# Optimization experiments

Hardware: AMD Instinct MI355X
Metric: run time of the kernel (lower is better)

## Reference

```python
import jax, jax.numpy as jnp
import numpy as np

EPS = 1e-5
NUM_HEADS = 8


def _conv_transpose_3x3_s2(x, w):
    # x: [B,Cin,H,W], w: [Cin,Cout,3,3] (torch ConvTranspose2d layout), stride 2, no padding
    # output spatial = (H-1)*2 + 3 = 2H+1
    return jax.lax.conv_transpose(
        x, w, strides=(2, 2), padding='VALID',
        dimension_numbers=('NCHW', 'IOHW', 'NCHW'))


def setup_inputs() -> dict:
    key = jax.random.key(0)
    ks = jax.random.split(key, 8)
    B, C, H, W = 4, 256, 32, 32
    Co, Dk, Dv = 128, 64, 64
    s = 0.05
    return {
        'x': jax.random.normal(ks[0], (B, C, H, W), jnp.float32),
        'gamma': jnp.ones((C,), jnp.float32),
        'beta': jnp.zeros((C,), jnp.float32),
        'running_mean': jax.random.normal(ks[1], (C,), jnp.float32) * 0.1,
        'running_var': jax.random.uniform(ks[2], (C,), jnp.float32, 0.5, 1.5),
        'w_sc': jax.random.normal(ks[3], (C, Co, 3, 3), jnp.float32) * s,
        'w_q': jax.random.normal(ks[4], (C, Dk, 3, 3), jnp.float32) * s,
        'w_k': jax.random.normal(ks[5], (Dk, C), jnp.float32) * s,
        'w_v': jax.random.normal(ks[6], (Dv, C), jnp.float32) * s,
        'w_o': jax.random.normal(ks[7], (Co, Dv), jnp.float32) * s,
    }


def reference(x, gamma, beta, running_mean, running_var, w_sc, w_q, w_k, w_v, w_o):
    B, C, H, W = x.shape
    h = NUM_HEADS
    # BatchNorm (inference, running stats) + ReLU, shared by both branches
    inv = jax.lax.rsqrt(running_var + EPS)
    xn = (x - running_mean[None, :, None, None]) * (gamma * inv)[None, :, None, None] \
         + beta[None, :, None, None]
    xr = jax.nn.relu(xn)

    # Shortcut: ConvTranspose2d(C->Co, 3, stride 2) -> [B,Co,2H+1,2W+1]
    shortcut = _conv_transpose_3x3_s2(xr, w_sc)

    # Attention branch ('UP'): query upsampled via ConvTranspose, k/v 1x1 at low res
    q = _conv_transpose_3x3_s2(xr, w_q)              # [B,Dk,Hu,Wu]
    k = jnp.einsum('dc,bchw->bdhw', w_k, xr)         # [B,Dk,H,W]
    v = jnp.einsum('dc,bchw->bdhw', w_v, xr)         # [B,Dv,H,W]
    Hu, Wu = q.shape[2], q.shape[3]
    Nq, Nk = Hu * Wu, H * W
    Dk, Dv = q.shape[1], v.shape[1]
    dk = Dk // h
    qh = q.reshape(B, h, dk, Nq)
    kh = k.reshape(B, h, dk, Nk)
    vh = v.reshape(B, h, Dv // h, Nk)
    scores = jnp.einsum('bhdq,bhdk->bhqk', qh, kh) / jnp.sqrt(jnp.float32(dk))
    attn = jax.nn.softmax(scores, axis=-1)           # use_softmax=True
    out = jnp.einsum('bhqk,bhdk->bhdq', attn, vh)    # [B,h,dv,Nq]
    out = out.reshape(B, Dv, Hu, Wu)
    out = jnp.einsum('od,bdhw->bohw', w_o, out)      # 1x1 output projection -> Co

    return shortcut + out
```

## Files before the change

kernel.cpp:

```cpp
#include <hip/hip_runtime.h>

typedef unsigned short u16;
typedef unsigned int u32;

typedef float f4 __attribute__((ext_vector_type(4)));
typedef short s8v __attribute__((ext_vector_type(8)));
typedef u16 us8 __attribute__((ext_vector_type(8)));
typedef _Float16 h4 __attribute__((ext_vector_type(4)));
typedef __fp16 g2 __attribute__((ext_vector_type(2)));

__device__ __forceinline__ u16 f2bf(float x){ u32 b=__float_as_uint(x); b += 0x7FFFu + ((b>>16)&1u); return (u16)(b>>16); }
__device__ __forceinline__ u16 f2h(float x){ union{_Float16 h; u16 u;} c; c.h=(_Float16)x; return c.u; }

#define O_XRT  4096u
#define O_WPT  (O_XRT + 2367488u)
#define O_QH   (O_WPT + 884736u)
#define O_KT   (O_QH  + 2163200u)
#define O_V    (O_KT  + 524288u)
#define O_ATT  (O_V   + 524288u)
#define O_WKV  (O_ATT + 2163200u)
#define O_WO2  (O_WKV + 65536u)

__global__ __launch_bounds__(256) void k_prep(
    const float* __restrict__ x, const float* __restrict__ gamma, const float* __restrict__ beta,
    const float* __restrict__ mean, const float* __restrict__ var,
    const float* __restrict__ w_sc, const float* __restrict__ w_q,
    const float* __restrict__ w_k, const float* __restrict__ w_v, const float* __restrict__ w_o,
    u16* __restrict__ xrTp, u16* __restrict__ wpt,
    u16* __restrict__ wkv, u16* __restrict__ wo2)
{
  __shared__ float SS[128], SH[128];
  __shared__ __align__(16) u16 T[32*136];
  int bi = blockIdx.x, tid = threadIdx.x;
  if (bi < 256) {
    int b = bi >> 6, pt = (bi >> 1) & 31, ch = bi & 1;
    int pix0 = pt*32, c0 = ch*128;
    if (tid < 128) {
      int c = c0 + tid;
      float s = gamma[c]*rsqrtf(var[c] + 1e-5f);
      SS[tid] = s; SH[tid] = beta[c] - mean[c]*s;
    }
    __syncthreads();
    int pix_l = tid & 31, c_l = tid >> 5;
    #pragma unroll 4
    for (int it = 0; it < 16; ++it) {
      int cl = it*8 + c_l;
      float v = x[(((size_t)(b*256 + c0 + cl))<<10) + pix0 + pix_l];
      T[pix_l*136 + cl] = f2bf(fmaxf(v*SS[cl] + SH[cl], 0.f));
    }
    __syncthreads();
    int pix_r = tid >> 3, j = tid & 7;
    us8 v0 = *(const us8*)(T + pix_r*136 + j*8);
    us8 v1 = *(const us8*)(T + pix_r*136 + 64 + j*8);
    u16* dst = xrTp + (((size_t)(b*1156 + (pt+1)*34 + 1 + pix_r))<<8) + c0;
    *(us8*)(dst + j*8) = v0;
    *(us8*)(dst + 64 + j*8) = v1;
    return;
  }
  int wid = (bi - 256)*256 + tid;
  if (wid < 442368) {
    int c, m, ky, kx; float val;
    if (wid < 294912) {
      c = wid / 1152; int r = wid - c*1152; m = r / 9; int t9 = r - m*9; ky = t9/3; kx = t9 - ky*3;
      val = w_sc[wid];
    } else {
      int i2 = wid - 294912;
      c = i2 / 576; int r = i2 - c*576; m = r / 9; int t9 = r - m*9; ky = t9/3; kx = t9 - ky*3;
      val = w_q[i2] * 0.51007023f;
      m += 128;
    }
    int py = (ky==1) ? 1 : 0; int dy = (ky==0) ? 1 : 0;
    int px = (kx==1) ? 1 : 0; int dx = (kx==0) ? 1 : 0;
    int cls = py*2 + px;
    int tt, KP, base;
    if (cls==0){ tt = dy*2+dx; KP=1024; base=0; }
    else if (cls==1){ tt = dy; KP=512; base=196608; }
    else if (cls==2){ tt = dx; KP=512; base=294912; }
    else { tt = 0; KP=256; base=393216; }
    wpt[base + m*KP + tt*256 + c] = f2bf(val);
  } else if (wid < 475136) {
    int i = wid - 442368; int m = i >> 8, c = i & 255;
    float vv = (m < 64) ? w_k[m*256 + c] : w_v[(m-64)*256 + c];
    wkv[m*256 + c] = f2bf(vv);
  } else if (wid < 483328) {
    int i = wid - 475136;
    wo2[i] = f2bf(w_o[i]);
  } else if (wid < 500224) {
    int i = wid - 483328;
    int b = i / 4224; int r = i - b*4224;
    int hp = r >> 5, j = r & 31;
    int p;
    if (hp < 34) p = hp;
    else if (hp < 68) p = 33*34 + (hp - 34);
    else if (hp < 100) p = (hp - 68 + 1)*34;
    else p = (hp - 100 + 1)*34 + 33;
    *(us8*)(xrTp + (((size_t)(b*1156 + p))<<8) + j*8) = (us8)0;
  }
}

template<int PY,int PX,int TT>
__device__ __forceinline__ void conv_cls(
    const u16* __restrict__ xrTp, const u16* __restrict__ wcls,
    float* __restrict__ outF, u16* __restrict__ qh,
    int mb, int nb, u16* Blds)
{
  constexpr int Hy = 33 - PY, Wx = 33 - PX;
  constexpr int NC = 4*Hy*Wx;
  constexpr int KP = TT*256;
  constexpr int NKT = KP/64;
  int tid = threadIdx.x;
  int lane = tid & 63, wv = tid >> 6, quad = lane >> 4, c15 = lane & 15;
  int sn = tid >> 2, sg = tid & 3;
  int n_g = nb*64 + sn;
  int ncl = n_g < NC ? n_g : NC-1;
  int bb = ncl/(Hy*Wx); int rem = ncl - bb*(Hy*Wx); int yq = rem/Wx; int xq = rem - yq*Wx;
  const u16* bsrc = xrTp + (((size_t)(bb*1156 + (yq+1)*34 + xq+1))<<8) + sg*16;
  f4 acc[4];
  #pragma unroll
  for (int i=0;i<4;i++) acc[i] = (f4){0.f,0.f,0.f,0.f};
  const u16* arow = wcls + (size_t)(mb*64 + wv*16 + c15)*KP + quad*8;
  auto loadB = [&](int kt, us8& v0, us8& v1) {
    int tt = kt >> 2, c0 = (kt & 3)*64;
    int dy, dx;
    if (TT==4){ dy = tt>>1; dx = tt&1; }
    else if (TT==2){ if (PX==1){ dy=tt; dx=0; } else { dy=0; dx=tt; } }
    else { dy=0; dx=0; }
    const u16* p = bsrc - (((dy*34+dx))<<8) + c0;
    v0 = *(const us8*)p;
    v1 = *(const us8*)(p+8);
  };
  us8 cv0, cv1; loadB(0, cv0, cv1);
  int pb = 0;
  for (int kt = 0; kt < NKT; ++kt) {
    u16* Bw = Blds + pb*4608;
    *(us8*)(Bw + sn*72 + sg*16) = cv0;
    *(us8*)(Bw + sn*72 + sg*16 + 8) = cv1;
    __syncthreads();
    if (kt + 1 < NKT) loadB(kt+1, cv0, cv1);
    s8v a0 = *(const s8v*)(arow + kt*64);
    s8v a1 = *(const s8v*)(arow + kt*64 + 32);
    #pragma unroll
    for (int t4=0;t4<4;t4++) {
      const u16* br = Blds + pb*4608 + (t4*16 + c15)*72 + quad*8;
      s8v bf0 = *(const s8v*)br;
      s8v bf1 = *(const s8v*)(br + 32);
      acc[t4] = __builtin_amdgcn_mfma_f32_16x16x32_bf16(a0, bf0, acc[t4], 0, 0, 0);
      acc[t4] = __builtin_amdgcn_mfma_f32_16x16x32_bf16(a1, bf1, acc[t4], 0, 0, 0);
    }
    pb ^= 1;
  }
  #pragma unroll
  for (int t4=0;t4<4;t4++) {
    int n2 = nb*64 + t4*16 + c15;
    if (n2 < NC) {
      int bb2 = n2/(Hy*Wx); int rem2 = n2 - bb2*(Hy*Wx); int yq2 = rem2/Wx; int xq2 = rem2 - yq2*Wx;
      int pix = (2*yq2 + PY)*65 + (2*xq2 + PX);
      if (mb < 2) {
        int mrow = mb*64 + wv*16 + quad*4;
        #pragma unroll
        for (int rg=0; rg<4; rg++)
          outF[(size_t)(bb2*128 + mrow + rg)*4225 + pix] = acc[t4][rg];
      } else {
        int dv = wv*16 + quad*4;
        u16 pk[4];
        #pragma unroll
        for (int rg=0; rg<4; rg++) pk[rg] = f2h(acc[t4][rg]);
        *(uint2*)(qh + (((size_t)(bb2*4225 + pix))<<6) + dv) = *(uint2*)pk;
      }
    }
  }
}

__global__ __launch_bounds__(256) void k_conv(
    const u16* __restrict__ xrTp, const u16* __restrict__ wpt, const u16* __restrict__ wkv,
    float* __restrict__ outF, u16* __restrict__ qh,
    u16* __restrict__ kT, u16* __restrict__ vbuf)
{
  __shared__ __align__(16) u16 Blds[2*4608];
  int bi = blockIdx.x;
  if (bi < 795) {
    int mb = bi % 3, cy = bi / 3;
    if (cy < 69)       conv_cls<0,0,4>(xrTp, wpt,          outF, qh, mb, cy,     Blds);
    else if (cy < 135) conv_cls<0,1,2>(xrTp, wpt + 196608, outF, qh, mb, cy-69,  Blds);
    else if (cy < 201) conv_cls<1,0,2>(xrTp, wpt + 294912, outF, qh, mb, cy-135, Blds);
    else               conv_cls<1,1,1>(xrTp, wpt + 393216, outF, qh, mb, cy-201, Blds);
    return;
  }
  int t = bi - 795;
  int mb = t & 1, nb = t >> 1;
  int tid = threadIdx.x;
  int lane = tid & 63, wv = tid >> 6, quad = lane >> 4, c15 = lane & 15;
  int sn = tid >> 2, sg = tid & 3;
  int n_g = nb*64 + sn;
  int b0 = n_g >> 10, pix0 = n_g & 1023, y0 = pix0 >> 5, x0 = pix0 & 31;
  const u16* bsrc = xrTp + (((size_t)(b0*1156 + (y0+1)*34 + x0+1))<<8) + sg*16;
  f4 acc[4];
  #pragma unroll
  for (int i=0;i<4;i++) acc[i] = (f4){0.f,0.f,0.f,0.f};
  const u16* arow = wkv + (size_t)(mb*64 + wv*16 + c15)*256 + quad*8;
  us8 cv0 = *(const us8*)bsrc, cv1 = *(const us8*)(bsrc + 8);
  int pb = 0;
  for (int kt = 0; kt < 4; ++kt) {
    u16* Bw = Blds + pb*4608;
    *(us8*)(Bw + sn*72 + sg*16) = cv0;
    *(us8*)(Bw + sn*72 + sg*16 + 8) = cv1;
    __syncthreads();
    if (kt < 3) { cv0 = *(const us8*)(bsrc + (kt+1)*64); cv1 = *(const us8*)(bsrc + (kt+1)*64 + 8); }
    s8v a0 = *(const s8v*)(arow + kt*64);
    s8v a1 = *(const s8v*)(arow + kt*64 + 32);
    #pragma unroll
    for (int t4=0;t4<4;t4++) {
      const u16* br = Blds + pb*4608 + (t4*16 + c15)*72 + quad*8;
      s8v bf0 = *(const s8v*)br;
      s8v bf1 = *(const s8v*)(br + 32);
      acc[t4] = __builtin_amdgcn_mfma_f32_16x16x32_bf16(a0, bf0, acc[t4], 0, 0, 0);
      acc[t4] = __builtin_amdgcn_mfma_f32_16x16x32_bf16(a1, bf1, acc[t4], 0, 0, 0);
    }
    pb ^= 1;
  }
  int ml = wv*16 + quad*4;
  #pragma unroll
  for (int t4=0;t4<4;t4++) {
    int n2 = nb*64 + t4*16 + c15;
    int b = n2 >> 10, pix = n2 & 1023;
    if (mb == 0) {
      int h = ml >> 3, d0 = ml & 7;
      u16 pk[4];
      #pragma unroll
      for (int rg=0; rg<4; rg++) pk[rg] = f2h(acc[t4][rg]);
      *(uint2*)(kT + ((size_t)(b*8+h)<<13) + pix*8 + d0) = *(uint2*)pk;
    } else {
      #pragma unroll
      for (int rg=0; rg<4; rg++)
        vbuf[(((size_t)(b*64 + ml + rg))<<10) + pix] = f2h(acc[t4][rg]);
    }
  }
}

__global__ __launch_bounds__(256) void k_attn(
    const u16* __restrict__ qh, const u16* __restrict__ kT, const u16* __restrict__ vbuf,
    u16* __restrict__ attT)
{
  __shared__ __align__(16) u16 KL[8192];
  __shared__ __align__(16) u16 VL[9*1032];
  int qt = blockIdx.x, bh = blockIdx.y;
  int b = bh >> 3, h = bh & 7;
  int tid = threadIdx.x, lane = tid & 63, wv = tid >> 6, quad = lane >> 4, c15 = lane & 15;
  {
    const uint4* kg = (const uint4*)(kT + ((size_t)bh << 13));
    for (int i = tid; i < 1024; i += 256) ((uint4*)KL)[i] = kg[i];
    const u16* vg = vbuf + ((size_t)(b*64 + h*8) << 10);
    for (int i = tid; i < 1024; i += 256) {
      int dv = i >> 7, k8 = (i & 127) << 3;
      *(uint4*)(VL + dv*1032 + k8) = *(const uint4*)(vg + (dv<<10) + k8);
    }
    if (tid < 129) {
      us8 ones;
      #pragma unroll
      for (int i=0;i<8;i++) ones[i] = 0x3C00;
      *(us8*)(VL + 8*1032 + tid*8) = ones;
    }
  }
  __syncthreads();
  int q0 = qt*128 + wv*32 + c15;
  int q1 = q0 + 16;
  int qa = q0 < 4224 ? q0 : 4224;
  int qb = q1 < 4224 ? q1 : 4224;
  uint2 t0 = *(const uint2*)(qh + (((size_t)(b*4225 + qa))<<6) + h*8 + (quad&1)*4);
  uint2 t1 = *(const uint2*)(qh + (((size_t)(b*4225 + qb))<<6) + h*8 + (quad&1)*4);
  h4 bq0 = quad < 2 ? *(h4*)&t0 : (h4)(_Float16)0.f;
  h4 bq1 = quad < 2 ? *(h4*)&t1 : (h4)(_Float16)0.f;
  const u16* klb = KL + c15*8 + (quad&1)*4;
  int vr = c15 > 8 ? 8 : c15;
  const u16* vlb = VL + vr*1032 + quad*4;
  const f4 zf = {0.f,0.f,0.f,0.f};
  f4 O0 = {0.f,0.f,0.f,0.f}, O1 = {0.f,0.f,0.f,0.f};
  union HU { uint2 u; h4 h; };
  #pragma unroll 8
  for (int kt=0; kt<64; ++kt) {
    h4 ak = *(const h4*)(klb + kt*128);
    h4 av = *(const h4*)(vlb + kt*16);
    f4 s0 = __builtin_amdgcn_mfma_f32_16x16x16f16(ak, bq0, zf, 0, 0, 0);
    f4 s1 = __builtin_amdgcn_mfma_f32_16x16x16f16(ak, bq1, zf, 0, 0, 0);
    g2 p0l = __builtin_amdgcn_cvt_pkrtz(__builtin_amdgcn_exp2f(s0[0]), __builtin_amdgcn_exp2f(s0[1]));
    g2 p0h = __builtin_amdgcn_cvt_pkrtz(__builtin_amdgcn_exp2f(s0[2]), __builtin_amdgcn_exp2f(s0[3]));
    g2 p1l = __builtin_amdgcn_cvt_pkrtz(__builtin_amdgcn_exp2f(s1[0]), __builtin_amdgcn_exp2f(s1[1]));
    g2 p1h = __builtin_amdgcn_cvt_pkrtz(__builtin_amdgcn_exp2f(s1[2]), __builtin_amdgcn_exp2f(s1[3]));
    HU u0; u0.u.x = __builtin_bit_cast(u32, p0l); u0.u.y = __builtin_bit_cast(u32, p0h);
    HU u1; u1.u.x = __builtin_bit_cast(u32, p1l); u1.u.y = __builtin_bit_cast(u32, p1h);
    O0 = __builtin_amdgcn_mfma_f32_16x16x16f16(av, u0.h, O0, 0, 0, 0);
    O1 = __builtin_amdgcn_mfma_f32_16x16x16f16(av, u1.h, O1, 0, 0, 0);
  }
  float l0 = __shfl(O0[0], 32 + c15, 64);
  float l1 = __shfl(O1[0], 32 + c15, 64);
  float r0 = __builtin_amdgcn_rcpf(l0);
  float r1 = __builtin_amdgcn_rcpf(l1);
  if (quad < 2) {
    if (q0 < 4225) {
      u16 pk[4];
      #pragma unroll
      for (int rg=0;rg<4;rg++) pk[rg] = f2bf(O0[rg]*r0);
      *(uint2*)(attT + (((size_t)(b*4225 + q0))<<6) + h*8 + quad*4) = *(uint2*)pk;
    }
    if (q1 < 4225) {
      u16 pk[4];
      #pragma unroll
      for (int rg=0;rg<4;rg++) pk[rg] = f2bf(O1[rg]*r1);
      *(uint2*)(attT + (((size_t)(b*4225 + q1))<<6) + h*8 + quad*4) = *(uint2*)pk;
    }
  }
}

__global__ __launch_bounds__(256) void k_proj(
    const u16* __restrict__ attT, const u16* __restrict__ wo2, float* __restrict__ outF)
{
  int nbi = blockIdx.x, b = blockIdx.y;
  int tid = threadIdx.x;
  int lane = tid & 63, wv = tid >> 6, quad = lane >> 4, c15 = lane & 15;
  f4 acc[2][4];
  #pragma unroll
  for (int am=0;am<2;am++)
    #pragma unroll
    for (int i=0;i<4;i++) acc[am][i] = (f4){0.f,0.f,0.f,0.f};
  #pragma unroll
  for (int kt = 0; kt < 2; ++kt) {
    s8v a0 = *(const s8v*)(wo2 + (size_t)(wv*32 + c15)*64 + kt*32 + quad*8);
    s8v a1 = *(const s8v*)(wo2 + (size_t)(wv*32 + 16 + c15)*64 + kt*32 + quad*8);
    #pragma unroll
    for (int t4=0;t4<4;t4++) {
      int n = nbi*64 + t4*16 + c15;
      int nc = n < 4224 ? n : 4224;
      s8v bf = *(const s8v*)(attT + (((size_t)(b*4225 + nc))<<6) + kt*32 + quad*8);
      acc[0][t4] = __builtin_amdgcn_mfma_f32_16x16x32_bf16(a0, bf, acc[0][t4], 0, 0, 0);
      acc[1][t4] = __builtin_amdgcn_mfma_f32_16x16x32_bf16(a1, bf, acc[1][t4], 0, 0, 0);
    }
  }
  #pragma unroll
  for (int am=0;am<2;am++) {
    int mrow = wv*32 + am*16 + quad*4;
    #pragma unroll
    for (int t4=0;t4<4;t4++) {
      int n2 = nbi*64 + t4*16 + c15;
      if (n2 < 4225) {
        float* op = outF + (size_t)(b*128 + mrow)*4225 + n2;
        #pragma unroll
        for (int rg=0; rg<4; rg++) op[(size_t)rg*4225] += acc[am][t4][rg];
      }
    }
  }
}

extern "C" void kernel_launch(void* const* d_in, const int* in_sizes, int n_in,
                              void* d_out, int out_size, void* d_ws, size_t ws_size,
                              hipStream_t stream) {
  const float* x     = (const float*)d_in[0];
  const float* gamma = (const float*)d_in[1];
  const float* beta  = (const float*)d_in[2];
  const float* mean  = (const float*)d_in[3];
  const float* var   = (const float*)d_in[4];
  const float* w_sc  = (const float*)d_in[5];
  const float* w_q   = (const float*)d_in[6];
  const float* w_k   = (const float*)d_in[7];
  const float* w_v   = (const float*)d_in[8];
  const float* w_o   = (const float*)d_in[9];
  char* ws = (char*)d_ws;
  u16*   xrTp = (u16*)(ws + O_XRT);
  u16*   wpt  = (u16*)(ws + O_WPT);
  u16*   qhb  = (u16*)(ws + O_QH);
  u16*   kT   = (u16*)(ws + O_KT);
  u16*   vbuf = (u16*)(ws + O_V);
  u16*   attT = (u16*)(ws + O_ATT);
  u16*   wkv  = (u16*)(ws + O_WKV);
  u16*   wo2  = (u16*)(ws + O_WO2);
  float* outF = (float*)d_out;

  k_prep<<<2211, 256, 0, stream>>>(x, gamma, beta, mean, var, w_sc, w_q, w_k, w_v, w_o,
                                   xrTp, wpt, wkv, wo2);
  k_conv<<<923, 256, 0, stream>>>(xrTp, wpt, wkv, outF, qhb, kT, vbuf);
  k_attn<<<dim3(34, 32), 256, 0, stream>>>(qhb, kT, vbuf, attT);
  k_proj<<<dim3(67, 4), 256, 0, stream>>>(attT, wo2, outF);
}
```

Before: 135.5 us.

## Widen per-block M tiles in conv/kv GEMMs and query tile in attention

The conv kernel now makes each block compute all three 64-row M slices (shortcut, shortcut, query) for one N tile, and the k/v projection computes both k and v per block. This reuses the shared-memory B tile across M and prefetches A fragments one step ahead. The attention kernel processes 4 query sub-tiles per wave instead of 2, halving the grid, and the prep kernel splits channels into 4 groups to double block count. The trade is fewer blocks and higher register pressure in exchange for less redundant B-tile loading and better MFMA density per barrier.

```diff
diff --git a/kernel.cpp b/kernel.cpp
--- a/kernel.cpp
+++ b/kernel.cpp
@@ -29,35 +29,33 @@
     u16* __restrict__ xrTp, u16* __restrict__ wpt,
     u16* __restrict__ wkv, u16* __restrict__ wo2)
 {
-  __shared__ float SS[128], SH[128];
-  __shared__ __align__(16) u16 T[32*136];
+  __shared__ float SS[64], SH[64];
+  __shared__ __align__(16) u16 T[32*72];
   int bi = blockIdx.x, tid = threadIdx.x;
-  if (bi < 256) {
-    int b = bi >> 6, pt = (bi >> 1) & 31, ch = bi & 1;
-    int pix0 = pt*32, c0 = ch*128;
-    if (tid < 128) {
+  if (bi < 512) {
+    int b = bi >> 7, pt = (bi >> 2) & 31, ch = bi & 3;
+    int pix0 = pt*32, c0 = ch*64;
+    if (tid < 64) {
       int c = c0 + tid;
       float s = gamma[c]*rsqrtf(var[c] + 1e-5f);
       SS[tid] = s; SH[tid] = beta[c] - mean[c]*s;
     }
     __syncthreads();
     int pix_l = tid & 31, c_l = tid >> 5;
-    #pragma unroll 4
-    for (int it = 0; it < 16; ++it) {
+    #pragma unroll
+    for (int it = 0; it < 8; ++it) {
       int cl = it*8 + c_l;
       float v = x[(((size_t)(b*256 + c0 + cl))<<10) + pix0 + pix_l];
-      T[pix_l*136 + cl] = f2bf(fmaxf(v*SS[cl] + SH[cl], 0.f));
+      T[pix_l*72 + cl] = f2bf(fmaxf(v*SS[cl] + SH[cl], 0.f));
     }
     __syncthreads();
     int pix_r = tid >> 3, j = tid & 7;
-    us8 v0 = *(const us8*)(T + pix_r*136 + j*8);
-    us8 v1 = *(const us8*)(T + pix_r*136 + 64 + j*8);
+    us8 v0 = *(const us8*)(T + pix_r*72 + j*8);
     u16* dst = xrTp + (((size_t)(b*1156 + (pt+1)*34 + 1 + pix_r))<<8) + c0;
     *(us8*)(dst + j*8) = v0;
-    *(us8*)(dst + 64 + j*8) = v1;
     return;
   }
-  int wid = (bi - 256)*256 + tid;
+  int wid = (bi - 512)*256 + tid;
   if (wid < 442368) {
     int c, m, ky, kx; float val;
     if (wid < 294912) {
@@ -102,7 +100,7 @@
 __device__ __forceinline__ void conv_cls(
     const u16* __restrict__ xrTp, const u16* __restrict__ wcls,
     float* __restrict__ outF, u16* __restrict__ qh,
-    int mb, int nb, u16* Blds)
+    int nb, u16* Blds)
 {
   constexpr int Hy = 33 - PY, Wx = 33 - PX;
   constexpr int NC = 4*Hy*Wx;
@@ -115,10 +113,14 @@
   int ncl = n_g < NC ? n_g : NC-1;
   int bb = ncl/(Hy*Wx); int rem = ncl - bb*(Hy*Wx); int yq = rem/Wx; int xq = rem - yq*Wx;
   const u16* bsrc = xrTp + (((size_t)(bb*1156 + (yq+1)*34 + xq+1))<<8) + sg*16;
-  f4 acc[4];
-  #pragma unroll
-  for (int i=0;i<4;i++) acc[i] = (f4){0.f,0.f,0.f,0.f};
-  const u16* arow = wcls + (size_t)(mb*64 + wv*16 + c15)*KP + quad*8;
+  f4 acc[3][4];
+  #pragma unroll
+  for (int s=0;s<3;s++)
+    #pragma unroll
+    for (int i=0;i<4;i++) acc[s][i] = (f4){0.f,0.f,0.f,0.f};
+  const u16* arow[3];
+  #pragma unroll
+  for (int s=0;s<3;s++) arow[s] = wcls + (size_t)(s*64 + wv*16 + c15)*KP + quad*8;
   auto loadB = [&](int kt, us8& v0, us8& v1) {
     int tt = kt >> 2, c0 = (kt & 3)*64;
     int dy, dx;
@@ -130,22 +132,33 @@
     v1 = *(const us8*)(p+8);
   };
   us8 cv0, cv1; loadB(0, cv0, cv1);
+  s8v a0[3], a1[3];
+  #pragma unroll
+  for (int s=0;s<3;s++) { a0[s] = *(const s8v*)(arow[s]); a1[s] = *(const s8v*)(arow[s] + 32); }
   int pb = 0;
   for (int kt = 0; kt < NKT; ++kt) {
     u16* Bw = Blds + pb*4608;
     *(us8*)(Bw + sn*72 + sg*16) = cv0;
     *(us8*)(Bw + sn*72 + sg*16 + 8) = cv1;
     __syncthreads();
-    if (kt + 1 < NKT) loadB(kt+1, cv0, cv1);
-    s8v a0 = *(const s8v*)(arow + kt*64);
-    s8v a1 = *(const s8v*)(arow + kt*64 + 32);
+    s8v u0[3], u1[3];
+    #pragma unroll
+    for (int s=0;s<3;s++){ u0[s]=a0[s]; u1[s]=a1[s]; }
+    if (kt + 1 < NKT) {
+      loadB(kt+1, cv0, cv1);
+      #pragma unroll
+      for (int s=0;s<3;s++) { a0[s] = *(const s8v*)(arow[s] + (kt+1)*64); a1[s] = *(const s8v*)(arow[s] + (kt+1)*64 + 32); }
+    }
     #pragma unroll
     for (int t4=0;t4<4;t4++) {
       const u16* br = Blds + pb*4608 + (t4*16 + c15)*72 + quad*8;
       s8v bf0 = *(const s8v*)br;
       s8v bf1 = *(const s8v*)(br + 32);
-      acc[t4] = __builtin_amdgcn_mfma_f32_16x16x32_bf16(a0, bf0, acc[t4], 0, 0, 0);
-      acc[t4] = __builtin_amdgcn_mfma_f32_16x16x32_bf16(a1, bf1, acc[t4], 0, 0, 0);
+      #pragma unroll
+      for (int s=0;s<3;s++) {
+        acc[s][t4] = __builtin_amdgcn_mfma_f32_16x16x32_bf16(u0[s], bf0, acc[s][t4], 0, 0, 0);
+        acc[s][t4] = __builtin_amdgcn_mfma_f32_16x16x32_bf16(u1[s], bf1, acc[s][t4], 0, 0, 0);
+      }
     }
     pb ^= 1;
   }
@@ -155,18 +168,18 @@
     if (n2 < NC) {
       int bb2 = n2/(Hy*Wx); int rem2 = n2 - bb2*(Hy*Wx); int yq2 = rem2/Wx; int xq2 = rem2 - yq2*Wx;
       int pix = (2*yq2 + PY)*65 + (2*xq2 + PX);
-      if (mb < 2) {
-        int mrow = mb*64 + wv*16 + quad*4;
+      #pragma unroll
+      for (int s=0;s<2;s++) {
+        int mrow = s*64 + wv*16 + quad*4;
         #pragma unroll
         for (int rg=0; rg<4; rg++)
-          outF[(size_t)(bb2*128 + mrow + rg)*4225 + pix] = acc[t4][rg];
-      } else {
-        int dv = wv*16 + quad*4;
-        u16 pk[4];
-        #pragma unroll
-        for (int rg=0; rg<4; rg++) pk[rg] = f2h(acc[t4][rg]);
-        *(uint2*)(qh + (((size_t)(bb2*4225 + pix))<<6) + dv) = *(uint2*)pk;
+          outF[(size_t)(bb2*128 + mrow + rg)*4225 + pix] = acc[s][t4][rg];
       }
+      int dv = wv*16 + quad*4;
+      u16 pk[4];
+      #pragma unroll
+      for (int rg=0; rg<4; rg++) pk[rg] = f2h(acc[2][t4][rg]);
+      *(uint2*)(qh + (((size_t)(bb2*4225 + pix))<<6) + dv) = *(uint2*)pk;
     }
   }
 }
@@ -178,43 +191,57 @@
 {
   __shared__ __align__(16) u16 Blds[2*4608];
   int bi = blockIdx.x;
-  if (bi < 795) {
-    int mb = bi % 3, cy = bi / 3;
-    if (cy < 69)       conv_cls<0,0,4>(xrTp, wpt,          outF, qh, mb, cy,     Blds);
-    else if (cy < 135) conv_cls<0,1,2>(xrTp, wpt + 196608, outF, qh, mb, cy-69,  Blds);
-    else if (cy < 201) conv_cls<1,0,2>(xrTp, wpt + 294912, outF, qh, mb, cy-135, Blds);
-    else               conv_cls<1,1,1>(xrTp, wpt + 393216, outF, qh, mb, cy-201, Blds);
+  if (bi < 265) {
+    int cy = bi;
+    if (cy < 69)       conv_cls<0,0,4>(xrTp, wpt,          outF, qh, cy,     Blds);
+    else if (cy < 135) conv_cls<0,1,2>(xrTp, wpt + 196608, outF, qh, cy-69,  Blds);
+    else if (cy < 201) conv_cls<1,0,2>(xrTp, wpt + 294912, outF, qh, cy-135, Blds);
+    else               conv_cls<1,1,1>(xrTp, wpt + 393216, outF, qh, cy-201, Blds);
     return;
   }
-  int t = bi - 795;
-  int mb = t & 1, nb = t >> 1;
+  int nb = bi - 265;
   int tid = threadIdx.x;
   int lane = tid & 63, wv = tid >> 6, quad = lane >> 4, c15 = lane & 15;
   int sn = tid >> 2, sg = tid & 3;
   int n_g = nb*64 + sn;
   int b0 = n_g >> 10, pix0 = n_g & 1023, y0 = pix0 >> 5, x0 = pix0 & 31;
   const u16* bsrc = xrTp + (((size_t)(b0*1156 + (y0+1)*34 + x0+1))<<8) + sg*16;
-  f4 acc[4];
-  #pragma unroll
-  for (int i=0;i<4;i++) acc[i] = (f4){0.f,0.f,0.f,0.f};
-  const u16* arow = wkv + (size_t)(mb*64 + wv*16 + c15)*256 + quad*8;
+  f4 acc[2][4];
+  #pragma unroll
+  for (int s=0;s<2;s++)
+    #pragma unroll
+    for (int i=0;i<4;i++) acc[s][i] = (f4){0.f,0.f,0.f,0.f};
+  const u16* arow[2];
+  #pragma unroll
+  for (int s=0;s<2;s++) arow[s] = wkv + (size_t)(s*64 + wv*16 + c15)*256 + quad*8;
   us8 cv0 = *(const us8*)bsrc, cv1 = *(const us8*)(bsrc + 8);
+  s8v a0[2], a1[2];
+  #pragma unroll
+  for (int s=0;s<2;s++) { a0[s] = *(const s8v*)(arow[s]); a1[s] = *(const s8v*)(arow[s] + 32); }
   int pb = 0;
   for (int kt = 0; kt < 4; ++kt) {
     u16* Bw = Blds + pb*4608;
     *(us8*)(Bw + sn*72 + sg*16) = cv0;
     *(us8*)(Bw + sn*72 + sg*16 + 8) = cv1;
     __syncthreads();
-    if (kt < 3) { cv0 = *(const us8*)(bsrc + (kt+1)*64); cv1 = *(const us8*)(bsrc + (kt+1)*64 + 8); }
-    s8v a0 = *(const s8v*)(arow + kt*64);
-    s8v a1 = *(const s8v*)(arow + kt*64 + 32);
+    s8v u0[2], u1[2];
+    #pragma unroll
+    for (int s=0;s<2;s++){ u0[s]=a0[s]; u1[s]=a1[s]; }
+    if (kt < 3) {
+      cv0 = *(const us8*)(bsrc + (kt+1)*64); cv1 = *(const us8*)(bsrc + (kt+1)*64 + 8);
+      #pragma unroll
+      for (int s=0;s<2;s++) { a0[s] = *(const s8v*)(arow[s] + (kt+1)*64); a1[s] = *(const s8v*)(arow[s] + (kt+1)*64 + 32); }
+    }
     #pragma unroll
     for (int t4=0;t4<4;t4++) {
       const u16* br = Blds + pb*4608 + (t4*16 + c15)*72 + quad*8;
       s8v bf0 = *(const s8v*)br;
       s8v bf1 = *(const s8v*)(br + 32);
-      acc[t4] = __builtin_amdgcn_mfma_f32_16x16x32_bf16(a0, bf0, acc[t4], 0, 0, 0);
-      acc[t4] = __builtin_amdgcn_mfma_f32_16x16x32_bf16(a1, bf1, acc[t4], 0, 0, 0);
+      #pragma unroll
+      for (int s=0;s<2;s++) {
+        acc[s][t4] = __builtin_amdgcn_mfma_f32_16x16x32_bf16(u0[s], bf0, acc[s][t4], 0, 0, 0);
+        acc[s][t4] = __builtin_amdgcn_mfma_f32_16x16x32_bf16(u1[s], bf1, acc[s][t4], 0, 0, 0);
+      }
     }
     pb ^= 1;
   }
@@ -223,16 +250,17 @@
   for (int t4=0;t4<4;t4++) {
     int n2 = nb*64 + t4*16 + c15;
     int b = n2 >> 10, pix = n2 & 1023;
-    if (mb == 0) {
+    {
       int h = ml >> 3, d0 = ml & 7;
       u16 pk[4];
       #pragma unroll
-      for (int rg=0; rg<4; rg++) pk[rg] = f2h(acc[t4][rg]);
+      for (int rg=0; rg<4; rg++) pk[rg] = f2h(acc[0][t4][rg]);
       *(uint2*)(kT + ((size_t)(b*8+h)<<13) + pix*8 + d0) = *(uint2*)pk;
-    } else {
+    }
+    {
       #pragma unroll
       for (int rg=0; rg<4; rg++)
-        vbuf[(((size_t)(b*64 + ml + rg))<<10) + pix] = f2h(acc[t4][rg]);
+        vbuf[(((size_t)(b*64 + ml + rg))<<10) + pix] = f2h(acc[1][t4][rg]);
     }
   }
 }
@@ -262,51 +290,44 @@
     }
   }
   __syncthreads();
-  int q0 = qt*128 + wv*32 + c15;
-  int q1 = q0 + 16;
-  int qa = q0 < 4224 ? q0 : 4224;
-  int qb = q1 < 4224 ? q1 : 4224;
-  uint2 t0 = *(const uint2*)(qh + (((size_t)(b*4225 + qa))<<6) + h*8 + (quad&1)*4);
-  uint2 t1 = *(const uint2*)(qh + (((size_t)(b*4225 + qb))<<6) + h*8 + (quad&1)*4);
-  h4 bq0 = quad < 2 ? *(h4*)&t0 : (h4)(_Float16)0.f;
-  h4 bq1 = quad < 2 ? *(h4*)&t1 : (h4)(_Float16)0.f;
+  int qv[4]; h4 bq[4];
+  #pragma unroll
+  for (int j=0;j<4;j++) {
+    qv[j] = qt*256 + wv*64 + j*16 + c15;
+    int qa = qv[j] < 4224 ? qv[j] : 4224;
+    uint2 t = *(const uint2*)(qh + (((size_t)(b*4225 + qa))<<6) + h*8 + (quad&1)*4);
+    bq[j] = quad < 2 ? *(h4*)&t : (h4)(_Float16)0.f;
+  }
   const u16* klb = KL + c15*8 + (quad&1)*4;
   int vr = c15 > 8 ? 8 : c15;
   const u16* vlb = VL + vr*1032 + quad*4;
   const f4 zf = {0.f,0.f,0.f,0.f};
-  f4 O0 = {0.f,0.f,0.f,0.f}, O1 = {0.f,0.f,0.f,0.f};
+  f4 O[4];
+  #pragma unroll
+  for (int j=0;j<4;j++) O[j] = (f4){0.f,0.f,0.f,0.f};
   union HU { uint2 u; h4 h; };
-  #pragma unroll 8
+  #pragma unroll 4
   for (int kt=0; kt<64; ++kt) {
     h4 ak = *(const h4*)(klb + kt*128);
     h4 av = *(const h4*)(vlb + kt*16);
-    f4 s0 = __builtin_amdgcn_mfma_f32_16x16x16f16(ak, bq0, zf, 0, 0, 0);
-    f4 s1 = __builtin_amdgcn_mfma_f32_16x16x16f16(ak, bq1, zf, 0, 0, 0);
-    g2 p0l = __builtin_amdgcn_cvt_pkrtz(__builtin_amdgcn_exp2f(s0[0]), __builtin_amdgcn_exp2f(s0[1]));
-    g2 p0h = __builtin_amdgcn_cvt_pkrtz(__builtin_amdgcn_exp2f(s0[2]), __builtin_amdgcn_exp2f(s0[3]));
-    g2 p1l = __builtin_amdgcn_cvt_pkrtz(__builtin_amdgcn_exp2f(s1[0]), __builtin_amdgcn_exp2f(s1[1]));
-    g2 p1h = __builtin_amdgcn_cvt_pkrtz(__builtin_amdgcn_exp2f(s1[2]), __builtin_amdgcn_exp2f(s1[3]));
-    HU u0; u0.u.x = __builtin_bit_cast(u32, p0l); u0.u.y = __builtin_bit_cast(u32, p0h);
-    HU u1; u1.u.x = __builtin_bit_cast(u32, p1l); u1.u.y = __builtin_bit_cast(u32, p1h);
-    O0 = __builtin_amdgcn_mfma_f32_16x16x16f16(av, u0.h, O0, 0, 0, 0);
-    O1 = __builtin_amdgcn_mfma_f32_16x16x16f16(av, u1.h, O1, 0, 0, 0);
-  }
-  float l0 = __shfl(O0[0], 32 + c15, 64);
-  float l1 = __shfl(O1[0], 32 + c15, 64);
-  float r0 = __builtin_amdgcn_rcpf(l0);
-  float r1 = __builtin_amdgcn_rcpf(l1);
-  if (quad < 2) {
-    if (q0 < 4225) {
+    #pragma unroll
+    for (int j=0;j<4;j++) {
+      f4 s = __builtin_amdgcn_mfma_f32_16x16x16f16(ak, bq[j], zf, 0, 0, 0);
+      g2 pl = __builtin_amdgcn_cvt_pkrtz(__builtin_amdgcn_exp2f(s[0]), __builtin_amdgcn_exp2f(s[1]));
+      g2 ph = __builtin_amdgcn_cvt_pkrtz(__builtin_amdgcn_exp2f(s[2]), __builtin_amdgcn_exp2f(s[3]));
+      HU u; u.u.x = __builtin_bit_cast(u32, pl); u.u.y = __builtin_bit_cast(u32, ph);
+      O[j] = __builtin_amdgcn_mfma_f32_16x16x16f16(av, u.h, O[j], 0, 0, 0);
+    }
+  }
+  #pragma unroll
+  for (int j=0;j<4;j++) {
+    float l = __shfl(O[j][0], 32 + c15, 64);
+    float r = __builtin_amdgcn_rcpf(l);
+    if (quad < 2 && qv[j] < 4225) {
       u16 pk[4];
       #pragma unroll
-      for (int rg=0;rg<4;rg++) pk[rg] = f2bf(O0[rg]*r0);
-      *(uint2*)(attT + (((size_t)(b*4225 + q0))<<6) + h*8 + quad*4) = *(uint2*)pk;
-    }
-    if (q1 < 4225) {
-      u16 pk[4];
-      #pragma unroll
-      for (int rg=0;rg<4;rg++) pk[rg] = f2bf(O1[rg]*r1);
-      *(uint2*)(attT + (((size_t)(b*4225 + q1))<<6) + h*8 + quad*4) = *(uint2*)pk;
+      for (int rg=0;rg<4;rg++) pk[rg] = f2bf(O[j][rg]*r);
+      *(uint2*)(attT + (((size_t)(b*4225 + qv[j]))<<6) + h*8 + quad*4) = *(uint2*)pk;
     }
   }
 }
@@ -374,9 +395,9 @@
   u16*   wo2  = (u16*)(ws + O_WO2);
   float* outF = (float*)d_out;
 
-  k_prep<<<2211, 256, 0, stream>>>(x, gamma, beta, mean, var, w_sc, w_q, w_k, w_v, w_o,
+  k_prep<<<2466, 256, 0, stream>>>(x, gamma, beta, mean, var, w_sc, w_q, w_k, w_v, w_o,
                                    xrTp, wpt, wkv, wo2);
-  k_conv<<<923, 256, 0, stream>>>(xrTp, wpt, wkv, outF, qhb, kT, vbuf);
-  k_attn<<<dim3(34, 32), 256, 0, stream>>>(qhb, kT, vbuf, attT);
+  k_conv<<<329, 256, 0, stream>>>(xrTp, wpt, wkv, outF, qhb, kT, vbuf);
+  k_attn<<<dim3(17, 32), 256, 0, stream>>>(qhb, kT, vbuf, attT);
   k_proj<<<dim3(67, 4), 256, 0, stream>>>(attT, wo2, outF);
 }
```

Result: slower. 145.9 us (+7.6%).
